# Performance work log

Measured on AMD Instinct MI355X. Metric: run time of the kernel, lower is better.

The kernel has to match this reference:

```python
import jax, jax.numpy as jnp
import numpy as np

NMS_SIGMA = 2.0
MASK_THRESH = 0.5
N = 500
H = W = 256
NUM_CLS = 80


def setup_inputs() -> dict:
    key = jax.random.key(0)
    k1, k2, k3 = jax.random.split(key, 3)
    mask_preds = jax.random.uniform(k1, (N, H, W), dtype=jnp.float32)
    cate_scores = jax.random.uniform(k2, (N,), dtype=jnp.float32)
    cate_labels = jax.random.randint(k3, (N,), 0, NUM_CLS, dtype=jnp.int32)
    return {"mask_preds": mask_preds, "cate_scores": cate_scores, "cate_labels": cate_labels}


def reference(mask_preds, cate_scores, cate_labels):
    n = mask_preds.shape[0]
    # binarize masks (SOLOv2 inference: seg_masks = seg_preds > mask_thresh)
    seg_masks = (mask_preds > MASK_THRESH).astype(mask_preds.dtype)  # [N,H,W]
    sum_masks = seg_masks.sum(axis=(1, 2))                           # [N]
    # mask scoring: average soft score inside the binary mask
    seg_scores = (mask_preds * seg_masks).sum(axis=(1, 2)) / jnp.maximum(sum_masks, 1.0)
    scores = cate_scores * seg_scores                                # [N]
    # sort descending by score (matrix-NMS assumes sorted order)
    order = jnp.argsort(-scores)
    scores = scores[order]
    labels = cate_labels[order]
    flat = seg_masks[order].reshape(n, -1)                           # [N,HW]
    sums = sum_masks[order]
    # pairwise mask IoU, upper-triangular (j suppressed by i<j)
    inter = flat @ flat.T                                            # [N,N]
    union = sums[:, None] + sums[None, :] - inter
    iou = jnp.triu(inter / jnp.maximum(union, 1.0), k=1)
    label_match = jnp.triu((labels[:, None] == labels[None, :]).astype(iou.dtype), k=1)
    decay_iou = iou * label_match                                    # [N,N]
    # gaussian matrix-NMS decay
    compensate_iou = decay_iou.max(axis=0)                           # [N]
    decay_matrix = jnp.exp(-NMS_SIGMA * (decay_iou ** 2 - compensate_iou[:, None] ** 2))
    coeff = decay_matrix.min(axis=0)                                 # [N]
    updated_scores = scores * coeff
    return updated_scores
```

## Files before the change

kernel.cpp:

```cpp
#include <hip/hip_runtime.h>
#include <cstdint>

typedef unsigned long long u64;

#define THRESH 0.5f
#define SIGMA 2.0f
#define TPB 64
#define NSPLIT 16
#define CST 66
#define MAXN 512

__device__ __forceinline__ bool better(float sa, int a, float sb, int b) {
    return (sa > sb) || (sa == sb && a < b);
}

__global__ __launch_bounds__(256) void k_pack(
    const float* __restrict__ preds, u64* __restrict__ packed,
    double* __restrict__ pssum, int* __restrict__ pcnt, int HW)
{
    const int task = blockIdx.x;
    const int i = task >> 2, sub = task & 3;
    const int seg = HW >> 2;
    const float* src = preds + (size_t)i * HW + (size_t)sub * seg;
    u64* dst = packed + (size_t)i * (HW >> 6) + (size_t)sub * (seg >> 6);
    const int tid = threadIdx.x;
    const int wave = tid >> 6, lane = tid & 63;
    double ssum = 0.0;
    int cnt = 0;
    const int iters = seg >> 12;
    for (int k = 0; k < iters; ++k) {
        const int base = (k << 12) + (wave << 10) + (lane << 2);
        const float4 v0 = *reinterpret_cast<const float4*>(src + base);
        const float4 v1 = *reinterpret_cast<const float4*>(src + base + 256);
        const float4 v2 = *reinterpret_cast<const float4*>(src + base + 512);
        const float4 v3 = *reinterpret_cast<const float4*>(src + base + 768);
        #pragma unroll
        for (int q = 0; q < 4; ++q) {
            const float4 v = (q == 0) ? v0 : (q == 1) ? v1 : (q == 2) ? v2 : v3;
            const bool b0 = v.x > THRESH, b1 = v.y > THRESH, b2 = v.z > THRESH, b3 = v.w > THRESH;
            const u64 m0 = __ballot(b0);
            const u64 m1 = __ballot(b1);
            const u64 m2 = __ballot(b2);
            const u64 m3 = __ballot(b3);
            if (lane < 4) {
                const u64 m = (lane == 0) ? m0 : (lane == 1) ? m1 : (lane == 2) ? m2 : m3;
                dst[(k << 6) + (wave << 4) + (q << 2) + lane] = m;
            }
            cnt += (int)b0 + (int)b1 + (int)b2 + (int)b3;
            ssum += (b0 ? (double)v.x : 0.0) + (b1 ? (double)v.y : 0.0)
                  + (b2 ? (double)v.z : 0.0) + (b3 ? (double)v.w : 0.0);
        }
    }
    for (int off = 32; off > 0; off >>= 1) {
        ssum += __shfl_down(ssum, off);
        cnt  += __shfl_down(cnt, off);
    }
    __shared__ double ls[4];
    __shared__ int lc[4];
    if (lane == 0) { ls[wave] = ssum; lc[wave] = cnt; }
    __syncthreads();
    if (tid == 0) {
        pssum[task] = ls[0] + ls[1] + ls[2] + ls[3];
        pcnt[task]  = lc[0] + lc[1] + lc[2] + lc[3];
    }
}

__global__ __launch_bounds__(256) void k_inter(
    const u64* __restrict__ packed, unsigned* __restrict__ part,
    int N, int WORDS, int NT)
{
    __shared__ __align__(16) u64 sm[2 * TPB][CST];
    int b = blockIdx.x;
    int ti = 0, rowlen = NT;
    while (b >= rowlen) { b -= rowlen; ++ti; --rowlen; }
    const int tj = ti + b;
    const int kwords = WORDS / NSPLIT;
    const int kbase = blockIdx.y * kwords;

    const int tid = threadIdx.x;
    const int a = tid >> 4, bb = tid & 15;

    const int half = kwords >> 1;
    for (int idx = tid; idx < 2 * TPB * half; idx += 256) {
        const int ml = idx / half;
        const int w = (idx - ml * half) << 1;
        const int g = (ml < TPB) ? (ti * TPB + ml) : (tj * TPB + (ml - TPB));
        u64 x0 = 0, x1 = 0;
        if (g < N) {
            const u64* p = packed + (size_t)g * WORDS + kbase + w;
            x0 = p[0];
            x1 = p[1];
        }
        sm[ml][w] = x0;
        sm[ml][w + 1] = x1;
    }
    __syncthreads();

    unsigned acc[4][4] = {};
    #pragma unroll 4
    for (int w = 0; w < kwords; w += 2) {
        u64 pi0[4], pi1[4], pj0[4], pj1[4];
        #pragma unroll
        for (int t = 0; t < 4; ++t) {
            const ulonglong2 q = *reinterpret_cast<const ulonglong2*>(&sm[4 * a + t][w]);
            pi0[t] = q.x; pi1[t] = q.y;
        }
        #pragma unroll
        for (int s = 0; s < 4; ++s) {
            const ulonglong2 q = *reinterpret_cast<const ulonglong2*>(&sm[TPB + bb + 16 * s][w]);
            pj0[s] = q.x; pj1[s] = q.y;
        }
        #pragma unroll
        for (int t = 0; t < 4; ++t)
            #pragma unroll
            for (int s = 0; s < 4; ++s)
                acc[t][s] += (unsigned)__popcll(pi0[t] & pj0[s])
                           + (unsigned)__popcll(pi1[t] & pj1[s]);
    }
    #pragma unroll
    for (int t = 0; t < 4; ++t)
        #pragma unroll
        for (int s = 0; s < 4; ++s) {
            const int gi = ti * TPB + 4 * a + t;
            const int gj = tj * TPB + bb + 16 * s;
            if (gj < N && gi < gj)
                part[((size_t)gi * N + gj) * NSPLIT + blockIdx.y] = acc[t][s];
        }
}

__device__ __forceinline__ unsigned fold16(const unsigned* __restrict__ p) {
    const uint4* q = reinterpret_cast<const uint4*>(p);
    unsigned s = 0;
    #pragma unroll
    for (int k = 0; k < 4; ++k) {
        const uint4 v = q[k];
        s += v.x + v.y + v.z + v.w;
    }
    return s;
}

__device__ __forceinline__ void finalize_scores(
    const double* __restrict__ pssum, const int* __restrict__ pcnt,
    const float* __restrict__ cate, const int* __restrict__ labels,
    float* s_score, float* s_sum, int* s_label, int N, int tid)
{
    for (int idx = tid; idx < N; idx += 256) {
        const double S = ((pssum[4*idx] + pssum[4*idx+1]) + pssum[4*idx+2]) + pssum[4*idx+3];
        const int C = ((pcnt[4*idx] + pcnt[4*idx+1]) + pcnt[4*idx+2]) + pcnt[4*idx+3];
        s_score[idx] = cate[idx] * (float)(S / (double)(C > 1 ? C : 1));
        s_sum[idx] = (float)C;
        s_label[idx] = labels[idx];
    }
    __syncthreads();
}

__global__ __launch_bounds__(256) void k_comp(
    const unsigned* __restrict__ part,
    const double* __restrict__ pssum, const int* __restrict__ pcnt,
    const float* __restrict__ cate, const int* __restrict__ labels,
    float* __restrict__ comp, int N)
{
    __shared__ float s_score[MAXN];
    __shared__ float s_sum[MAXN];
    __shared__ int s_label[MAXN];
    const int tid = threadIdx.x;
    finalize_scores(pssum, pcnt, cate, labels, s_score, s_sum, s_label, N, tid);

    const int bI = blockIdx.x;
    const float sb = s_score[bI], sub = s_sum[bI];
    const int lb = s_label[bI];
    float m = 0.0f;
    for (int a = tid; a < N; a += 256) {
        if (a == bI || s_label[a] != lb) continue;
        if (!better(s_score[a], a, sb, bI)) continue;
        const int lo = a < bI ? a : bI, hi = a < bI ? bI : a;
        const float inter = (float)fold16(part + ((size_t)lo * N + hi) * NSPLIT);
        const float un = s_sum[a] + sub - inter;
        m = fmaxf(m, inter / fmaxf(un, 1.0f));
    }
    for (int off = 32; off > 0; off >>= 1) m = fmaxf(m, __shfl_down(m, off));
    __shared__ float lm[4];
    const int wave = tid >> 6, lane = tid & 63;
    if (lane == 0) lm[wave] = m;
    __syncthreads();
    if (tid == 0) comp[bI] = fmaxf(fmaxf(lm[0], lm[1]), fmaxf(lm[2], lm[3]));
}

__global__ __launch_bounds__(256) void k_final(
    const unsigned* __restrict__ part,
    const double* __restrict__ pssum, const int* __restrict__ pcnt,
    const float* __restrict__ cate, const int* __restrict__ labels,
    const float* __restrict__ comp, float* __restrict__ out, int N)
{
    __shared__ float s_score[MAXN];
    __shared__ float s_sum[MAXN];
    __shared__ int s_label[MAXN];
    const int tid = threadIdx.x;
    finalize_scores(pssum, pcnt, cate, labels, s_score, s_sum, s_label, N, tid);

    const int bI = blockIdx.x;
    const float sb = s_score[bI], sub = s_sum[bI];
    const int lb = s_label[bI];
    float m = -3.0e38f;
    int r = 0;
    for (int a = tid; a < N; a += 256) {
        const bool bet = (a != bI) && better(s_score[a], a, sb, bI);
        r += (int)bet;
        float d = 0.0f;
        if (bet && s_label[a] == lb) {
            const int lo = a < bI ? a : bI, hi = a < bI ? bI : a;
            const float inter = (float)fold16(part + ((size_t)lo * N + hi) * NSPLIT);
            const float un = s_sum[a] + sub - inter;
            d = inter / fmaxf(un, 1.0f);
        }
        const float ca = comp[a];
        m = fmaxf(m, d * d - ca * ca);
    }
    for (int off = 32; off > 0; off >>= 1) {
        m = fmaxf(m, __shfl_down(m, off));
        r += __shfl_down(r, off);
    }
    __shared__ float lm[4];
    __shared__ int lr[4];
    const int wave = tid >> 6, lane = tid & 63;
    if (lane == 0) { lm[wave] = m; lr[wave] = r; }
    __syncthreads();
    if (tid == 0) {
        const float mm = fmaxf(fmaxf(lm[0], lm[1]), fmaxf(lm[2], lm[3]));
        const int rank = lr[0] + lr[1] + lr[2] + lr[3];
        out[rank] = sb * expf(-SIGMA * mm);
    }
}

extern "C" void kernel_launch(void* const* d_in, const int* in_sizes, int n_in,
                              void* d_out, int out_size, void* d_ws, size_t ws_size,
                              hipStream_t stream)
{
    const float* preds  = (const float*)d_in[0];
    const float* cate   = (const float*)d_in[1];
    const int*   labels = (const int*)d_in[2];
    float* out = (float*)d_out;

    const int N = in_sizes[1];
    const int HW = in_sizes[0] / N;
    const int WORDS = HW >> 6;

    char* ws = (char*)d_ws;
    size_t off = 0;
    auto take = [&](size_t bytes) -> void* {
        void* p = ws + off;
        off = (off + bytes + 255) & ~(size_t)255;
        return p;
    };
    u64*      packed = (u64*)     take((size_t)N * WORDS * sizeof(u64));
    double*   pssum  = (double*)  take((size_t)N * 4 * sizeof(double));
    int*      pcnt   = (int*)     take((size_t)N * 4 * sizeof(int));
    float*    comp   = (float*)   take((size_t)N * sizeof(float));
    unsigned* part   = (unsigned*)take((size_t)N * N * NSPLIT * sizeof(unsigned));
    (void)ws_size; (void)n_in; (void)out_size;

    k_pack<<<N * 4, 256, 0, stream>>>(preds, packed, pssum, pcnt, HW);

    const int NT = (N + TPB - 1) / TPB;
    dim3 grid(NT * (NT + 1) / 2, NSPLIT);
    k_inter<<<grid, 256, 0, stream>>>(packed, part, N, WORDS, NT);

    k_comp<<<N, 256, 0, stream>>>(part, pssum, pcnt, cate, labels, comp, N);

    k_final<<<N, 256, 0, stream>>>(part, pssum, pcnt, cate, labels, comp, out, N);
}
```

Before: 244.2 us.

## Compute intersections only for same-label pairs and fuse compensate via atomicMax

Replaces the dense tiled popcount all-pairs intersection kernel with a wave-per-pair kernel. It computes AND-popcounts only for pairs with i<j that share a label, which is about 1/80 of the pairs for random labels. The compensate IoU is now accumulated directly with atomicMax on float bits, removing the separate k_comp kernel and the 16-way split partial buffer. The trade-off is that each pair's wave streams both full packed masks from global/L2 memory with no shared-memory reuse, and the grid-stride loop iterates over all N^2 pair indices.

Measured after the change: 223.8 us. 1.09x faster.

```diff
diff --git a/kernel.cpp b/kernel.cpp
--- a/kernel.cpp
+++ b/kernel.cpp
@@ -5,25 +5,36 @@
 
 #define THRESH 0.5f
 #define SIGMA 2.0f
-#define TPB 64
-#define NSPLIT 16
-#define CST 66
 #define MAXN 512
 
 __device__ __forceinline__ bool better(float sa, int a, float sb, int b) {
     return (sa > sb) || (sa == sb && a < b);
 }
 
+__device__ __forceinline__ float fscore(
+    const double* __restrict__ pssum, const int* __restrict__ pcnt,
+    const float* __restrict__ cate, int idx, float* __restrict__ sumOut)
+{
+    const double S = ((pssum[4*idx] + pssum[4*idx+1]) + pssum[4*idx+2]) + pssum[4*idx+3];
+    const int C = ((pcnt[4*idx] + pcnt[4*idx+1]) + pcnt[4*idx+2]) + pcnt[4*idx+3];
+    *sumOut = (float)C;
+    return cate[idx] * (float)(S / (double)(C > 1 ? C : 1));
+}
+
 __global__ __launch_bounds__(256) void k_pack(
     const float* __restrict__ preds, u64* __restrict__ packed,
-    double* __restrict__ pssum, int* __restrict__ pcnt, int HW)
+    double* __restrict__ pssum, int* __restrict__ pcnt,
+    unsigned* __restrict__ compU, int HW)
 {
     const int task = blockIdx.x;
+    const int tid = threadIdx.x;
+    if (task == 0) {
+        for (int t = tid; t < MAXN; t += 256) compU[t] = 0u;
+    }
     const int i = task >> 2, sub = task & 3;
     const int seg = HW >> 2;
     const float* src = preds + (size_t)i * HW + (size_t)sub * seg;
     u64* dst = packed + (size_t)i * (HW >> 6) + (size_t)sub * (seg >> 6);
-    const int tid = threadIdx.x;
     const int wave = tid >> 6, lane = tid & 63;
     double ssum = 0.0;
     int cnt = 0;
@@ -65,138 +76,67 @@
     }
 }
 
-__global__ __launch_bounds__(256) void k_inter(
-    const u64* __restrict__ packed, unsigned* __restrict__ part,
-    int N, int WORDS, int NT)
-{
-    __shared__ __align__(16) u64 sm[2 * TPB][CST];
-    int b = blockIdx.x;
-    int ti = 0, rowlen = NT;
-    while (b >= rowlen) { b -= rowlen; ++ti; --rowlen; }
-    const int tj = ti + b;
-    const int kwords = WORDS / NSPLIT;
-    const int kbase = blockIdx.y * kwords;
-
-    const int tid = threadIdx.x;
-    const int a = tid >> 4, bb = tid & 15;
-
-    const int half = kwords >> 1;
-    for (int idx = tid; idx < 2 * TPB * half; idx += 256) {
-        const int ml = idx / half;
-        const int w = (idx - ml * half) << 1;
-        const int g = (ml < TPB) ? (ti * TPB + ml) : (tj * TPB + (ml - TPB));
-        u64 x0 = 0, x1 = 0;
-        if (g < N) {
-            const u64* p = packed + (size_t)g * WORDS + kbase + w;
-            x0 = p[0];
-            x1 = p[1];
-        }
-        sm[ml][w] = x0;
-        sm[ml][w + 1] = x1;
-    }
-    __syncthreads();
-
-    unsigned acc[4][4] = {};
-    #pragma unroll 4
-    for (int w = 0; w < kwords; w += 2) {
-        u64 pi0[4], pi1[4], pj0[4], pj1[4];
-        #pragma unroll
-        for (int t = 0; t < 4; ++t) {
-            const ulonglong2 q = *reinterpret_cast<const ulonglong2*>(&sm[4 * a + t][w]);
-            pi0[t] = q.x; pi1[t] = q.y;
-        }
-        #pragma unroll
-        for (int s = 0; s < 4; ++s) {
-            const ulonglong2 q = *reinterpret_cast<const ulonglong2*>(&sm[TPB + bb + 16 * s][w]);
-            pj0[s] = q.x; pj1[s] = q.y;
-        }
-        #pragma unroll
-        for (int t = 0; t < 4; ++t)
-            #pragma unroll
-            for (int s = 0; s < 4; ++s)
-                acc[t][s] += (unsigned)__popcll(pi0[t] & pj0[s])
-                           + (unsigned)__popcll(pi1[t] & pj1[s]);
-    }
-    #pragma unroll
-    for (int t = 0; t < 4; ++t)
-        #pragma unroll
-        for (int s = 0; s < 4; ++s) {
-            const int gi = ti * TPB + 4 * a + t;
-            const int gj = tj * TPB + bb + 16 * s;
-            if (gj < N && gi < gj)
-                part[((size_t)gi * N + gj) * NSPLIT + blockIdx.y] = acc[t][s];
-        }
-}
-
-__device__ __forceinline__ unsigned fold16(const unsigned* __restrict__ p) {
-    const uint4* q = reinterpret_cast<const uint4*>(p);
-    unsigned s = 0;
-    #pragma unroll
-    for (int k = 0; k < 4; ++k) {
-        const uint4 v = q[k];
-        s += v.x + v.y + v.z + v.w;
-    }
-    return s;
-}
-
-__device__ __forceinline__ void finalize_scores(
+__global__ __launch_bounds__(256) void k_pairs(
+    const u64* __restrict__ packed,
     const double* __restrict__ pssum, const int* __restrict__ pcnt,
     const float* __restrict__ cate, const int* __restrict__ labels,
-    float* s_score, float* s_sum, int* s_label, int N, int tid)
-{
-    for (int idx = tid; idx < N; idx += 256) {
-        const double S = ((pssum[4*idx] + pssum[4*idx+1]) + pssum[4*idx+2]) + pssum[4*idx+3];
-        const int C = ((pcnt[4*idx] + pcnt[4*idx+1]) + pcnt[4*idx+2]) + pcnt[4*idx+3];
-        s_score[idx] = cate[idx] * (float)(S / (double)(C > 1 ? C : 1));
-        s_sum[idx] = (float)C;
-        s_label[idx] = labels[idx];
-    }
-    __syncthreads();
-}
-
-__global__ __launch_bounds__(256) void k_comp(
-    const unsigned* __restrict__ part,
+    unsigned* __restrict__ inter, unsigned* __restrict__ compU,
+    int N, int WORDS)
+{
+    const int wid = (blockIdx.x << 2) + (threadIdx.x >> 6);
+    const int lane = threadIdx.x & 63;
+    const int nw = gridDim.x << 2;
+    const int NN = N * N;
+    int i = wid / N;
+    int j = wid - i * N;
+    for (int p = wid; p < NN; p += nw) {
+        if (j > i && labels[i] == labels[j]) {
+            const u64* A = packed + (size_t)i * WORDS;
+            const u64* B = packed + (size_t)j * WORDS;
+            unsigned acc = 0;
+            const int iters = WORDS >> 7;
+            #pragma unroll 2
+            for (int k = 0; k < iters; ++k) {
+                const int idx = (k << 7) + (lane << 1);
+                const ulonglong2 a = *reinterpret_cast<const ulonglong2*>(A + idx);
+                const ulonglong2 b = *reinterpret_cast<const ulonglong2*>(B + idx);
+                acc += (unsigned)__popcll(a.x & b.x) + (unsigned)__popcll(a.y & b.y);
+            }
+            #pragma unroll
+            for (int off = 32; off > 0; off >>= 1) acc += __shfl_down(acc, off);
+            if (lane == 0) {
+                inter[(size_t)i * N + j] = acc;
+                float smi, smj;
+                const float si = fscore(pssum, pcnt, cate, i, &smi);
+                const float sj = fscore(pssum, pcnt, cate, j, &smj);
+                const int w = better(si, i, sj, j) ? j : i;
+                const float un = (smi + smj) - (float)acc;
+                const float iou = (float)acc / fmaxf(un, 1.0f);
+                atomicMax(&compU[w], __float_as_uint(iou));
+            }
+        }
+        j += nw;
+        while (j >= N) { j -= N; ++i; }
+    }
+}
+
+__global__ __launch_bounds__(256) void k_final(
+    const unsigned* __restrict__ inter,
     const double* __restrict__ pssum, const int* __restrict__ pcnt,
     const float* __restrict__ cate, const int* __restrict__ labels,
-    float* __restrict__ comp, int N)
+    const unsigned* __restrict__ compU, float* __restrict__ out, int N)
 {
     __shared__ float s_score[MAXN];
     __shared__ float s_sum[MAXN];
     __shared__ int s_label[MAXN];
     const int tid = threadIdx.x;
-    finalize_scores(pssum, pcnt, cate, labels, s_score, s_sum, s_label, N, tid);
-
-    const int bI = blockIdx.x;
-    const float sb = s_score[bI], sub = s_sum[bI];
-    const int lb = s_label[bI];
-    float m = 0.0f;
-    for (int a = tid; a < N; a += 256) {
-        if (a == bI || s_label[a] != lb) continue;
-        if (!better(s_score[a], a, sb, bI)) continue;
-        const int lo = a < bI ? a : bI, hi = a < bI ? bI : a;
-        const float inter = (float)fold16(part + ((size_t)lo * N + hi) * NSPLIT);
-        const float un = s_sum[a] + sub - inter;
-        m = fmaxf(m, inter / fmaxf(un, 1.0f));
-    }
-    for (int off = 32; off > 0; off >>= 1) m = fmaxf(m, __shfl_down(m, off));
-    __shared__ float lm[4];
-    const int wave = tid >> 6, lane = tid & 63;
-    if (lane == 0) lm[wave] = m;
+    for (int idx = tid; idx < N; idx += 256) {
+        float sm;
+        s_score[idx] = fscore(pssum, pcnt, cate, idx, &sm);
+        s_sum[idx] = sm;
+        s_label[idx] = labels[idx];
+    }
     __syncthreads();
-    if (tid == 0) comp[bI] = fmaxf(fmaxf(lm[0], lm[1]), fmaxf(lm[2], lm[3]));
-}
-
-__global__ __launch_bounds__(256) void k_final(
-    const unsigned* __restrict__ part,
-    const double* __restrict__ pssum, const int* __restrict__ pcnt,
-    const float* __restrict__ cate, const int* __restrict__ labels,
-    const float* __restrict__ comp, float* __restrict__ out, int N)
-{
-    __shared__ float s_score[MAXN];
-    __shared__ float s_sum[MAXN];
-    __shared__ int s_label[MAXN];
-    const int tid = threadIdx.x;
-    finalize_scores(pssum, pcnt, cate, labels, s_score, s_sum, s_label, N, tid);
 
     const int bI = blockIdx.x;
     const float sb = s_score[bI], sub = s_sum[bI];
@@ -209,11 +149,11 @@
         float d = 0.0f;
         if (bet && s_label[a] == lb) {
             const int lo = a < bI ? a : bI, hi = a < bI ? bI : a;
-            const float inter = (float)fold16(part + ((size_t)lo * N + hi) * NSPLIT);
-            const float un = s_sum[a] + sub - inter;
-            d = inter / fmaxf(un, 1.0f);
+            const float in = (float)inter[(size_t)lo * N + hi];
+            const float un = s_sum[a] + sub - in;
+            d = in / fmaxf(un, 1.0f);
         }
-        const float ca = comp[a];
+        const float ca = __uint_as_float(compU[a]);
         m = fmaxf(m, d * d - ca * ca);
     }
     for (int off = 32; off > 0; off >>= 1) {
@@ -255,17 +195,14 @@
     u64*      packed = (u64*)     take((size_t)N * WORDS * sizeof(u64));
     double*   pssum  = (double*)  take((size_t)N * 4 * sizeof(double));
     int*      pcnt   = (int*)     take((size_t)N * 4 * sizeof(int));
-    float*    comp   = (float*)   take((size_t)N * sizeof(float));
-    unsigned* part   = (unsigned*)take((size_t)N * N * NSPLIT * sizeof(unsigned));
+    unsigned* compU  = (unsigned*)take((size_t)MAXN * sizeof(unsigned));
+    unsigned* inter  = (unsigned*)take((size_t)N * N * sizeof(unsigned));
     (void)ws_size; (void)n_in; (void)out_size;
 
-    k_pack<<<N * 4, 256, 0, stream>>>(preds, packed, pssum, pcnt, HW);
-
-    const int NT = (N + TPB - 1) / TPB;
-    dim3 grid(NT * (NT + 1) / 2, NSPLIT);
-    k_inter<<<grid, 256, 0, stream>>>(packed, part, N, WORDS, NT);
-
-    k_comp<<<N, 256, 0, stream>>>(part, pssum, pcnt, cate, labels, comp, N);
-
-    k_final<<<N, 256, 0, stream>>>(part, pssum, pcnt, cate, labels, comp, out, N);
-}
+    k_pack<<<N * 4, 256, 0, stream>>>(preds, packed, pssum, pcnt, compU, HW);
+
+    k_pairs<<<1024, 256, 0, stream>>>(packed, pssum, pcnt, cate, labels,
+                                      inter, compU, N, WORDS);
+
+    k_final<<<N, 256, 0, stream>>>(inter, pssum, pcnt, cate, labels, compU, out, N);
+}
```
